# Kernel tuning notes

Measured on AMD Instinct MI355X. Metric: run time of the kernel, lower is better.

The kernel has to match this reference:

```python
import jax, jax.numpy as jnp
import numpy as np

EMBED_DIM = 1024
PROJ_DIM = 128
B = 32
S = 1024


def setup_inputs() -> dict:
    key = jax.random.key(0)
    k1, k2, k3 = jax.random.split(key, 3)
    context = jax.random.normal(k1, (S, B, EMBED_DIM), jnp.float32)  # [seq, batch, embed]
    prior = jax.random.uniform(k2, (B, S), dtype=jnp.float32)
    padding_mask = jnp.zeros((B, S), jnp.int32)
    # xavier_uniform for proj_weight [2*proj_dim, embed_dim]
    bound = float(np.sqrt(6.0 / (2 * PROJ_DIM + EMBED_DIM)))
    proj_weight = jax.random.uniform(k3, (2 * PROJ_DIM, EMBED_DIM), jnp.float32, -bound, bound)
    proj_bias = jnp.zeros((2 * PROJ_DIM,), jnp.float32)
    return {"context": context, "prior": prior, "padding_mask": padding_mask,
            "proj_weight": proj_weight, "proj_bias": proj_bias}


def reference(context, prior, padding_mask, proj_weight, proj_bias):
    ctx = jnp.transpose(context, (1, 0, 2))  # [B, S, E]
    b, s, e = ctx.shape
    qk = ctx @ proj_weight.T + proj_bias  # [B, S, 2*proj_dim]
    query, key = jnp.split(qk, 2, axis=2)
    # neighbor scores (note: original divides by embed_dim, not proj_dim)
    fwd = jnp.sum(query[:, :-1] * key[:, 1:], axis=-1) / e    # [B, S-1]
    bwd = jnp.sum(query[:, 1:] * key[:, :-1], axis=-1) / e    # [B, S-1]
    ninf = jnp.full((b, 1), -jnp.inf, ctx.dtype)
    col0 = jnp.concatenate([fwd, ninf], axis=1)   # score[:, :, 0]
    col1 = jnp.concatenate([ninf, bwd], axis=1)   # score[:, :, 1]
    rolled_mask = jnp.roll(padding_mask, -1, axis=1)
    col0 = jnp.where(rolled_mask == 1, -jnp.inf, col0)
    prob = jax.nn.softmax(jnp.stack([col0, col1], axis=-1), axis=-1)  # [B, S, 2]
    # torch .roll with no dims flattens first -- replicate exactly
    shift_prob = jnp.roll(prob[:, :, 1].reshape(-1), -1).reshape(b, s)
    p = jnp.sqrt(prob[:, :, 0] * shift_prob + 1e-6)
    neighbor_attn = prior + (1 - prior) * p  # [B, S]
    log_prob = jnp.log(neighbor_attn)
    log_prob = jnp.where(rolled_mask == 1, 0.0, log_prob)
    # The two triangular bmms compute C[i,j] = sum_{k=i}^{j-1} log_prob[k] for j>i.
    # Equivalent O(S^2) form via exclusive prefix sum of log_prob[:, :-1].
    csp = jnp.concatenate([jnp.zeros((b, 1), ctx.dtype),
                           jnp.cumsum(log_prob[:, :-1], axis=1)], axis=1)  # [B, S]
    diff = csp[:, None, :] - csp[:, :, None]  # diff[b,i,j] = csp[j] - csp[i]
    upper = jnp.triu(diff, k=1)
    constituent_attn = jnp.exp(upper + jnp.swapaxes(upper, 1, 2))
    constituent_attn = jnp.where(jnp.eye(s, dtype=bool), 0.0, constituent_attn)
    return constituent_attn, neighbor_attn
```

## Files before the change

kernel.cpp:

```cpp
#include <hip/hip_runtime.h>
#include <hip/hip_bf16.h>
#include <math.h>

#define EMB 1024
#define BATCH 32
#define SEQ 1024
#define J2 256
#define BM 64
#define BN 256
#define BK 64
#define PSEL 0x07060302u

typedef __attribute__((ext_vector_type(8))) short short8;
typedef __attribute__((ext_vector_type(4))) float f32x4;
typedef const __attribute__((address_space(1))) void gvoid;
typedef __attribute__((address_space(3))) void lvoid;

__device__ __forceinline__ unsigned bcast(float f) {
    union { float f; unsigned u; } c; c.f = f; return c.u;
}
__device__ __forceinline__ unsigned pack_bf16(float f0, float f1) {
    return __builtin_amdgcn_perm(bcast(f1) + 0x8000u, bcast(f0) + 0x8000u, PSEL);
}

__global__ __launch_bounds__(256) void convw(const float* __restrict__ W,
                                             __hip_bfloat16* __restrict__ Wb) {
    int i = blockIdx.x * 256 + threadIdx.x;
    float4 v = ((const float4*)W)[i];
    __hip_bfloat16 h[4];
    h[0] = __float2bfloat16(v.x); h[1] = __float2bfloat16(v.y);
    h[2] = __float2bfloat16(v.z); h[3] = __float2bfloat16(v.w);
    *(short4*)&Wb[i * 4] = *(short4*)h;
}

__global__ __launch_bounds__(256) void gemm_mfma(const float* __restrict__ ctx,
                                                 const __hip_bfloat16* __restrict__ Wb,
                                                 const float* __restrict__ bias,
                                                 __hip_bfloat16* __restrict__ qkb) {
    __shared__ __align__(16) __hip_bfloat16 As[BM * BK];
    __shared__ __align__(16) __hip_bfloat16 Bs[BN * BK];
    const int t = threadIdx.x;
    const int lane = t & 63, w = t >> 6;
    const int m0 = blockIdx.x * BM;
    const int wn = w * 64;
    const int lm = lane & 15, lq = lane >> 4;

    f32x4 acc[4][4] = {};

    float bv[4];
    #pragma unroll
    for (int ni = 0; ni < 4; ni++) bv[ni] = bias[wn + ni * 16 + lm];

    const float4* ctx4 = (const float4*)ctx;

    for (int k0 = 0; k0 < EMB; k0 += BK) {
        #pragma unroll
        for (int c = 0; c < 8; c++) {
            int li = c * 256 + t;
            int row = li >> 3, k8 = li & 7;
            const __hip_bfloat16* g = Wb + (size_t)row * EMB + k0 + k8 * 8;
            __hip_bfloat16* l = &Bs[(c * 256 + w * 64) * 8];
            __builtin_amdgcn_global_load_lds((gvoid*)g, (lvoid*)l, 16, 0, 0);
        }
        const int k4 = k0 >> 2;
        #pragma unroll
        for (int c = 0; c < 2; c++) {
            int li = c * 256 + t;
            int row = li >> 3, k8 = li & 7;
            float4 v0 = ctx4[(size_t)(m0 + row) * 256 + k4 + k8 * 2];
            float4 v1 = ctx4[(size_t)(m0 + row) * 256 + k4 + k8 * 2 + 1];
            uint4 p;
            p.x = pack_bf16(v0.x, v0.y);
            p.y = pack_bf16(v0.z, v0.w);
            p.z = pack_bf16(v1.x, v1.y);
            p.w = pack_bf16(v1.z, v1.w);
            *(uint4*)&As[row * BK + k8 * 8] = p;
        }
        __syncthreads();
        #pragma unroll
        for (int kk = 0; kk < BK; kk += 32) {
            short8 af[4], bfr[4];
            #pragma unroll
            for (int i = 0; i < 4; i++) {
                af[i]  = *(const short8*)&As[(i * 16 + lm) * BK + kk + lq * 8];
                bfr[i] = *(const short8*)&Bs[(wn + i * 16 + lm) * BK + kk + lq * 8];
            }
            #pragma unroll
            for (int mi = 0; mi < 4; mi++)
                #pragma unroll
                for (int ni = 0; ni < 4; ni++)
                    acc[mi][ni] = __builtin_amdgcn_mfma_f32_16x16x32_bf16(
                        af[mi], bfr[ni], acc[mi][ni], 0, 0, 0);
        }
        __syncthreads();
    }

    #pragma unroll
    for (int mi = 0; mi < 4; mi++) {
        #pragma unroll
        for (int r = 0; r < 4; r++) {
            int m = m0 + mi * 16 + lq * 4 + r;
            int s = m >> 5, b = m & 31;
            __hip_bfloat16* orow = qkb + (size_t)((b << 10) + s) * J2;
            #pragma unroll
            for (int ni = 0; ni < 4; ni++) {
                int n = wn + ni * 16 + lm;
                orow[n] = __float2bfloat16(acc[mi][ni][r] + bv[ni]);
            }
        }
    }
}

__global__ __launch_bounds__(256) void scores(const __hip_bfloat16* __restrict__ qkb,
                                              float* __restrict__ fwd,
                                              float* __restrict__ bwd) {
    int wave = threadIdx.x >> 6, lane = threadIdx.x & 63;
    int idx = blockIdx.x * 4 + wave;
    int s = idx & (SEQ - 1);
    if (s == SEQ - 1) return;
    const unsigned* r0 = (const unsigned*)(qkb + (size_t)idx * J2);
    const unsigned* r1 = r0 + 128;
    unsigned q0 = r0[lane], k0 = r0[64 + lane];
    unsigned q1 = r1[lane], k1 = r1[64 + lane];
    float2 q0f = __bfloat1622float2(*(const __hip_bfloat162*)&q0);
    float2 k0f = __bfloat1622float2(*(const __hip_bfloat162*)&k0);
    float2 q1f = __bfloat1622float2(*(const __hip_bfloat162*)&q1);
    float2 k1f = __bfloat1622float2(*(const __hip_bfloat162*)&k1);
    float f = q0f.x * k1f.x + q0f.y * k1f.y;
    float w = q1f.x * k0f.x + q1f.y * k0f.y;
    #pragma unroll
    for (int off = 32; off; off >>= 1) {
        f += __shfl_xor(f, off);
        w += __shfl_xor(w, off);
    }
    if (lane == 0) {
        fwd[idx] = f * (1.f / 1024.f);
        bwd[idx] = w * (1.f / 1024.f);
    }
}

__global__ __launch_bounds__(1024) void neighbor(const float* __restrict__ fwd,
                                                 const float* __restrict__ bwd,
                                                 const float* __restrict__ prior,
                                                 const int* __restrict__ mask,
                                                 float* __restrict__ out_n,
                                                 float* __restrict__ csp) {
    int b = blockIdx.x, s = threadIdx.x;
    int lane = s & 63, w = s >> 6;
    __shared__ float p1s[SEQ];
    __shared__ float incl[SEQ];
    __shared__ float wsum[16];
    int base = b << 10;
    int rolled = mask[base + ((s + 1) & (SEQ - 1))];
    float c0 = (s < SEQ - 1) ? fwd[base + s] : -INFINITY;
    if (rolled) c0 = -INFINITY;
    float c1 = (s > 0) ? bwd[base + s - 1] : -INFINITY;
    float m = fmaxf(c0, c1);
    float e0 = expf(c0 - m), e1 = expf(c1 - m);
    float inv = 1.f / (e0 + e1);
    float p0 = e0 * inv, p1 = e1 * inv;
    p1s[s] = p1;
    __syncthreads();
    float shift = (s < SEQ - 1) ? p1s[s + 1] : 0.f;
    float p = sqrtf(p0 * shift + 1e-6f);
    float pr = prior[base + s];
    float na = pr + (1.f - pr) * p;
    out_n[base + s] = na;
    float lp = logf(na);
    if (rolled) lp = 0.f;
    float x = lp;
    #pragma unroll
    for (int off = 1; off < 64; off <<= 1) {
        float v = __shfl_up(x, off);
        if (lane >= off) x += v;
    }
    if (lane == 63) wsum[w] = x;
    __syncthreads();
    if (w == 0) {
        float v = (lane < 16) ? wsum[lane] : 0.f;
        #pragma unroll
        for (int off = 1; off < 16; off <<= 1) {
            float t2 = __shfl_up(v, off);
            if (lane >= off) v += t2;
        }
        if (lane < 16) wsum[lane] = v;
    }
    __syncthreads();
    float woff = (w > 0) ? wsum[w - 1] : 0.f;
    incl[s] = x + woff;
    __syncthreads();
    csp[base + s] = (s == 0) ? 0.f : incl[s - 1];
}

__global__ __launch_bounds__(256) void outk(const float* __restrict__ csp,
                                            float* __restrict__ out) {
    int bi = blockIdx.x;
    int b = bi >> 10, i = bi & (SEQ - 1);
    const float* crow = csp + (b << 10);
    float ci = crow[i];
    int t = threadIdx.x;
    float4 cj = ((const float4*)crow)[t];
    int j0 = t << 2;
    float4 r;
    {
        int j = j0 + 0;
        r.x = (j == i) ? 0.f : expf((j > i) ? (cj.x - ci) : (ci - cj.x));
        j = j0 + 1;
        r.y = (j == i) ? 0.f : expf((j > i) ? (cj.y - ci) : (ci - cj.y));
        j = j0 + 2;
        r.z = (j == i) ? 0.f : expf((j > i) ? (cj.z - ci) : (ci - cj.z));
        j = j0 + 3;
        r.w = (j == i) ? 0.f : expf((j > i) ? (cj.w - ci) : (ci - cj.w));
    }
    ((float4*)(out + (size_t)bi * SEQ))[t] = r;
}

extern "C" void kernel_launch(void* const* d_in, const int* in_sizes, int n_in,
                              void* d_out, int out_size, void* d_ws, size_t ws_size,
                              hipStream_t stream) {
    (void)in_sizes; (void)n_in; (void)out_size; (void)ws_size;
    const float* ctx   = (const float*)d_in[0];
    const float* prior = (const float*)d_in[1];
    const int*   mask  = (const int*)d_in[2];
    const float* W     = (const float*)d_in[3];
    const float* bias  = (const float*)d_in[4];
    float* out = (float*)d_out;
    float* ws  = (float*)d_ws;

    __hip_bfloat16* qkb = (__hip_bfloat16*)ws;
    float* fwd = ws + 4194304;
    float* bwd = fwd + 32768;
    float* csp = bwd + 32768;
    __hip_bfloat16* Wb = (__hip_bfloat16*)(csp + 32768);
    float* out_n = out + (size_t)BATCH * SEQ * SEQ;

    convw    <<<256, 256, 0, stream>>>(W, Wb);
    gemm_mfma<<<(BATCH * SEQ) / BM, 256, 0, stream>>>(ctx, Wb, bias, qkb);
    scores   <<<(BATCH * SEQ) / 4, 256, 0, stream>>>(qkb, fwd, bwd);
    neighbor <<<BATCH, 1024, 0, stream>>>(fwd, bwd, prior, mask, out_n, csp);
    outk     <<<BATCH * SEQ, 256, 0, stream>>>(csp, out);
}
```

Baseline: 268.7 us.

## Double-buffer GEMM LDS tiles with swizzle; batch 8 rows per outk block

The projection GEMM now double-buffers its A and B LDS tiles. It prefetches the next K-slice of context into registers and issues async global-to-LDS loads for the weights while MFMAs run on the current buffer. It also XOR-swizzles the LDS layout to reduce bank conflicts and replaces the per-iteration syncthreads with explicit waitcnt and barrier. The output kernel handles 8 rows per block with fast __expf, cutting block count and launch overhead, at some cost in exp precision.

```diff
diff --git a/kernel.cpp b/kernel.cpp
--- a/kernel.cpp
+++ b/kernel.cpp
@@ -9,6 +9,7 @@
 #define BM 64
 #define BN 256
 #define BK 64
+#define NIT (EMB / BK)
 #define PSEL 0x07060302u
 
 typedef __attribute__((ext_vector_type(8))) short short8;
@@ -37,8 +38,8 @@
                                                  const __hip_bfloat16* __restrict__ Wb,
                                                  const float* __restrict__ bias,
                                                  __hip_bfloat16* __restrict__ qkb) {
-    __shared__ __align__(16) __hip_bfloat16 As[BM * BK];
-    __shared__ __align__(16) __hip_bfloat16 Bs[BN * BK];
+    __shared__ __align__(16) __hip_bfloat16 As[2 * BM * BK];
+    __shared__ __align__(16) __hip_bfloat16 Bs[2 * BN * BK];
     const int t = threadIdx.x;
     const int lane = t & 63, w = t >> 6;
     const int m0 = blockIdx.x * BM;
@@ -52,38 +53,79 @@
     for (int ni = 0; ni < 4; ni++) bv[ni] = bias[wn + ni * 16 + lm];
 
     const float4* ctx4 = (const float4*)ctx;
-
-    for (int k0 = 0; k0 < EMB; k0 += BK) {
-        #pragma unroll
-        for (int c = 0; c < 8; c++) {
-            int li = c * 256 + t;
-            int row = li >> 3, k8 = li & 7;
-            const __hip_bfloat16* g = Wb + (size_t)row * EMB + k0 + k8 * 8;
-            __hip_bfloat16* l = &Bs[(c * 256 + w * 64) * 8];
-            __builtin_amdgcn_global_load_lds((gvoid*)g, (lvoid*)l, 16, 0, 0);
-        }
-        const int k4 = k0 >> 2;
-        #pragma unroll
-        for (int c = 0; c < 2; c++) {
-            int li = c * 256 + t;
-            int row = li >> 3, k8 = li & 7;
-            float4 v0 = ctx4[(size_t)(m0 + row) * 256 + k4 + k8 * 2];
-            float4 v1 = ctx4[(size_t)(m0 + row) * 256 + k4 + k8 * 2 + 1];
-            uint4 p;
-            p.x = pack_bf16(v0.x, v0.y);
-            p.y = pack_bf16(v0.z, v0.w);
-            p.z = pack_bf16(v1.x, v1.y);
-            p.w = pack_bf16(v1.z, v1.w);
-            *(uint4*)&As[row * BK + k8 * 8] = p;
-        }
-        __syncthreads();
+    const int ar0 = t >> 3, ak = t & 7;
+    const int ar1 = 32 + ar0;
+    const int as0 = (ak ^ (ar0 & 7)) * 8;
+    const int as1 = (ak ^ (ar1 & 7)) * 8;
+    const size_t abase0 = (size_t)(m0 + ar0) * 256 + ak * 2;
+    const size_t abase1 = (size_t)(m0 + ar1) * 256 + ak * 2;
+
+    #pragma unroll
+    for (int c = 0; c < 8; c++) {
+        int li = c * 256 + t, row = li >> 3;
+        int k8 = (li & 7) ^ (row & 7);
+        __builtin_amdgcn_global_load_lds(
+            (gvoid*)(Wb + (size_t)row * EMB + k8 * 8),
+            (lvoid*)&Bs[(c * 256 + w * 64) * 8], 16, 0, 0);
+    }
+    __builtin_amdgcn_sched_barrier(0);
+    float4 v0a = ctx4[abase0], v0b = ctx4[abase0 + 1];
+    float4 v1a = ctx4[abase1], v1b = ctx4[abase1 + 1];
+    {
+        uint4 p0, p1;
+        p0.x = pack_bf16(v0a.x, v0a.y); p0.y = pack_bf16(v0a.z, v0a.w);
+        p0.z = pack_bf16(v0b.x, v0b.y); p0.w = pack_bf16(v0b.z, v0b.w);
+        p1.x = pack_bf16(v1a.x, v1a.y); p1.y = pack_bf16(v1a.z, v1a.w);
+        p1.z = pack_bf16(v1b.x, v1b.y); p1.w = pack_bf16(v1b.z, v1b.w);
+        *(uint4*)&As[ar0 * BK + as0] = p0;
+        *(uint4*)&As[ar1 * BK + as1] = p1;
+    }
+    __builtin_amdgcn_sched_barrier(0);
+    v0a = ctx4[abase0 + 16]; v0b = ctx4[abase0 + 17];
+    v1a = ctx4[abase1 + 16]; v1b = ctx4[abase1 + 17];
+    asm volatile("s_waitcnt vmcnt(4) lgkmcnt(0)" ::: "memory");
+    __builtin_amdgcn_s_barrier();
+
+    for (int it = 0; it < NIT; ++it) {
+        const int cur = it & 1;
+        const __hip_bfloat16* Ac = As + cur * (BM * BK);
+        const __hip_bfloat16* Bc = Bs + cur * (BN * BK);
+        __hip_bfloat16* An = As + (cur ^ 1) * (BM * BK);
+        __hip_bfloat16* Bn = Bs + (cur ^ 1) * (BN * BK);
+        const bool stage = (it + 1 < NIT);
+        const bool pre   = (it + 2 < NIT);
+        if (stage) {
+            const int k0n = (it + 1) * BK;
+            #pragma unroll
+            for (int c = 0; c < 8; c++) {
+                int li = c * 256 + t, row = li >> 3;
+                int k8 = (li & 7) ^ (row & 7);
+                __builtin_amdgcn_global_load_lds(
+                    (gvoid*)(Wb + (size_t)row * EMB + k0n + k8 * 8),
+                    (lvoid*)&Bn[(c * 256 + w * 64) * 8], 16, 0, 0);
+            }
+            __builtin_amdgcn_sched_barrier(0);
+            uint4 p0, p1;
+            p0.x = pack_bf16(v0a.x, v0a.y); p0.y = pack_bf16(v0a.z, v0a.w);
+            p0.z = pack_bf16(v0b.x, v0b.y); p0.w = pack_bf16(v0b.z, v0b.w);
+            p1.x = pack_bf16(v1a.x, v1a.y); p1.y = pack_bf16(v1a.z, v1a.w);
+            p1.z = pack_bf16(v1b.x, v1b.y); p1.w = pack_bf16(v1b.z, v1b.w);
+            *(uint4*)&An[ar0 * BK + as0] = p0;
+            *(uint4*)&An[ar1 * BK + as1] = p1;
+            if (pre) {
+                const size_t ko = (size_t)(it + 2) * (BK / 4);
+                v0a = ctx4[abase0 + ko]; v0b = ctx4[abase0 + ko + 1];
+                v1a = ctx4[abase1 + ko]; v1b = ctx4[abase1 + ko + 1];
+            }
+        }
         #pragma unroll
         for (int kk = 0; kk < BK; kk += 32) {
+            const int off = ((((kk >> 5) << 2) + lq) ^ (lm & 7)) * 8;
             short8 af[4], bfr[4];
             #pragma unroll
             for (int i = 0; i < 4; i++) {
-                af[i]  = *(const short8*)&As[(i * 16 + lm) * BK + kk + lq * 8];
-                bfr[i] = *(const short8*)&Bs[(wn + i * 16 + lm) * BK + kk + lq * 8];
+                af[i]  = *(const short8*)&Ac[(i * 16 + lm) * BK + off];
+                bfr[i] = *(const short8*)&Bc[(wn + i * 16 + lm) * BK + off];
             }
             #pragma unroll
             for (int mi = 0; mi < 4; mi++)
@@ -92,7 +134,13 @@
                     acc[mi][ni] = __builtin_amdgcn_mfma_f32_16x16x32_bf16(
                         af[mi], bfr[ni], acc[mi][ni], 0, 0, 0);
         }
-        __syncthreads();
+        if (stage) {
+            if (pre)
+                asm volatile("s_waitcnt vmcnt(4) lgkmcnt(0)" ::: "memory");
+            else
+                asm volatile("s_waitcnt vmcnt(0) lgkmcnt(0)" ::: "memory");
+            __builtin_amdgcn_s_barrier();
+        }
     }
 
     #pragma unroll
@@ -194,25 +242,28 @@
 
 __global__ __launch_bounds__(256) void outk(const float* __restrict__ csp,
                                             float* __restrict__ out) {
-    int bi = blockIdx.x;
-    int b = bi >> 10, i = bi & (SEQ - 1);
+    int blk = blockIdx.x;
+    int b = blk >> 7, i0 = (blk & 127) << 3;
     const float* crow = csp + (b << 10);
-    float ci = crow[i];
     int t = threadIdx.x;
     float4 cj = ((const float4*)crow)[t];
     int j0 = t << 2;
-    float4 r;
-    {
-        int j = j0 + 0;
-        r.x = (j == i) ? 0.f : expf((j > i) ? (cj.x - ci) : (ci - cj.x));
-        j = j0 + 1;
-        r.y = (j == i) ? 0.f : expf((j > i) ? (cj.y - ci) : (ci - cj.y));
-        j = j0 + 2;
-        r.z = (j == i) ? 0.f : expf((j > i) ? (cj.z - ci) : (ci - cj.z));
-        j = j0 + 3;
-        r.w = (j == i) ? 0.f : expf((j > i) ? (cj.w - ci) : (ci - cj.w));
-    }
-    ((float4*)(out + (size_t)bi * SEQ))[t] = r;
+    float4* o4 = (float4*)(out + ((size_t)(b << 10) + i0) * SEQ) + t;
+    #pragma unroll
+    for (int r = 0; r < 8; r++) {
+        int i = i0 + r;
+        float ci = crow[i];
+        float4 v; float d;
+        d = (j0 + 0 > i) ? cj.x - ci : ci - cj.x;
+        v.x = (j0 + 0 == i) ? 0.f : __expf(d);
+        d = (j0 + 1 > i) ? cj.y - ci : ci - cj.y;
+        v.y = (j0 + 1 == i) ? 0.f : __expf(d);
+        d = (j0 + 2 > i) ? cj.z - ci : ci - cj.z;
+        v.z = (j0 + 2 == i) ? 0.f : __expf(d);
+        d = (j0 + 3 > i) ? cj.w - ci : ci - cj.w;
+        v.w = (j0 + 3 == i) ? 0.f : __expf(d);
+        o4[r * 256] = v;
+    }
 }
 
 extern "C" void kernel_launch(void* const* d_in, const int* in_sizes, int n_in,
@@ -238,5 +289,5 @@
     gemm_mfma<<<(BATCH * SEQ) / BM, 256, 0, stream>>>(ctx, Wb, bias, qkb);
     scores   <<<(BATCH * SEQ) / 4, 256, 0, stream>>>(qkb, fwd, bwd);
     neighbor <<<BATCH, 1024, 0, stream>>>(fwd, bwd, prior, mask, out_n, csp);
-    outk     <<<BATCH * SEQ, 256, 0, stream>>>(csp, out);
-}
+    outk     <<<(BATCH * SEQ) / 8, 256, 0, stream>>>(csp, out);
+}
```

Measured after the change: 269.2 us. Within noise of the previous version (+0.2%).
